# Kernel optimization log

Measured on AMD Instinct MI355X. Metric: run time of the kernel, lower is better.

The kernel has to match this reference:

```python
import jax, jax.numpy as jnp
import numpy as np

B, H, W, C_IN, C_HID = 32, 64, 64, 384, 128

def setup_inputs() -> dict:
    key = jax.random.key(0)
    k0, k1, k2 = jax.random.split(key, 3)
    dino_features = jax.random.normal(k0, (B, H, W, C_IN), dtype=jnp.float32)
    # Xavier-uniform(gain=0.5) bounds for conv weights, HWIO layout
    fan1 = C_IN * 9 + C_HID * 9
    lim1 = 0.5 * np.sqrt(6.0 / fan1)
    W1 = jax.random.uniform(k1, (3, 3, C_IN, C_HID), minval=-lim1, maxval=lim1, dtype=jnp.float32)
    b1 = jnp.zeros((C_HID,), dtype=jnp.float32)
    fan2 = C_HID + 1
    lim2 = 0.5 * np.sqrt(6.0 / fan2)
    W2 = jax.random.uniform(k2, (1, 1, C_HID, 1), minval=-lim2, maxval=lim2, dtype=jnp.float32)
    b2 = jnp.zeros((1,), dtype=jnp.float32)
    return {"dino_features": dino_features, "W1": W1, "b1": b1, "W2": W2, "b2": b2}

def _conv(x, w, pad):
    # x: NHWC, w: HWIO -> NHWC
    return jax.lax.conv_general_dilated(
        x, w, window_strides=(1, 1), padding=pad,
        dimension_numbers=("NHWC", "HWIO", "NHWC"))

def reference(dino_features, W1, b1, W2, b2):
    # conv3x3 (pad 1) -> ReLU -> conv1x1 -> sigmoid; output (B,H,W,1)
    h = jax.nn.relu(_conv(dino_features, W1, ((1, 1), (1, 1))) + b1)
    logits = _conv(h, W2, ((0, 0), (0, 0))) + b2
    return jax.nn.sigmoid(logits)
```

## Files before the change

kernel.cpp:

```cpp
#include <hip/hip_runtime.h>
#include <math.h>


typedef __attribute__((ext_vector_type(8))) unsigned short ushort8;
typedef __attribute__((ext_vector_type(8))) __bf16 bf16x8;
typedef __attribute__((ext_vector_type(4))) float floatx4;

static __device__ __forceinline__ unsigned short f2bf(float f) {
  union { float f; unsigned int u; } x; x.f = f;
  return (unsigned short)((x.u + 0x8000u) >> 16);
}
static __device__ __forceinline__ unsigned short f2bf_rne(float f) {
  union { float f; unsigned int u; } x; x.f = f;
  unsigned int u = x.u;
  return (unsigned short)((u + 0x7fffu + ((u >> 16) & 1u)) >> 16);
}

__global__ void prep_w1_kernel(const float* __restrict__ W1,
                               unsigned short* __restrict__ W1b) {
  __shared__ unsigned short tile[32 * 128];
  const int kk = blockIdx.x;
  const int o = kk / 12;
  const int chunk = kk - o * 12;
  const float* src = W1 + (o * 384 + chunk * 32) * 128;
  const int t = threadIdx.x;
#pragma unroll
  for (int i = 0; i < 16; ++i) {
    int idx = t + i * 256;
    int c = idx >> 7;
    int n = idx & 127;
    tile[n * 32 + c] = f2bf_rne(src[idx]);
  }
  __syncthreads();
  unsigned short* dst = W1b + kk * 4096;
#pragma unroll
  for (int i = 0; i < 16; ++i) {
    int idx = t + i * 256;
    dst[idx] = tile[idx];
  }
}

__global__ __launch_bounds__(256) void conv_fused_kernel(
    const float* __restrict__ x, const unsigned short* __restrict__ W1b,
    const float* __restrict__ b1, const float* __restrict__ W2,
    const float* __restrict__ b2, float* __restrict__ out) {
  __shared__ alignas(16) unsigned short Ah[100 * 40];
  __shared__ float hsum[64 * 4];

  const int t = threadIdx.x;
  const int w = t >> 6;
  const int lane = t & 63;
  const int g = lane >> 4;
  const int lr = lane & 15;

  const int img = blockIdx.x >> 6;
  const int tileId = blockIdx.x & 63;
  const int ty0 = (tileId >> 3) << 3;
  const int tx0 = (tileId & 7) << 3;

  const int px0 = t >> 2, sub0 = t & 3;
  const int hy0 = (px0 * 205) >> 11;
  const int hx0 = px0 - hy0 * 10;
  const int iy0 = ty0 + hy0 - 1, ix0 = tx0 + hx0 - 1;
  const bool v0 = ((unsigned)iy0 < 64u) && ((unsigned)ix0 < 64u);
  const float* ab0 =
      x + ((((img << 6) + iy0) << 6) + ix0) * 384 + sub0 * 8;

  const int i1 = t + 256;
  const bool act1 = i1 < 400;
  const int px1 = i1 >> 2, sub1 = i1 & 3;
  const int hy1 = (px1 * 205) >> 11;
  const int hx1 = px1 - hy1 * 10;
  const int iy1 = ty0 + hy1 - 1, ix1 = tx0 + hx1 - 1;
  const bool v1 = act1 && ((unsigned)iy1 < 64u) && ((unsigned)ix1 < 64u);
  const float* ab1 =
      x + ((((img << 6) + iy1) << 6) + ix1) * 384 + sub1 * 8;

  const int boff = ((w * 32 + lr) << 5) + (g << 3);
  const int aoffb = ((lr >> 3) * 10 + (lr & 7)) * 40 + (g << 3);

  floatx4 acc[4][2] = {};

  const float b1v0 = b1[w * 32 + lr];
  const float b1v1 = b1[w * 32 + 16 + lr];
  const float w2v0 = W2[w * 32 + lr];
  const float w2v1 = W2[w * 32 + 16 + lr];

  for (int chunk = 0; chunk < 12; ++chunk) {
    ushort8 a0 = (ushort8)0, a1 = (ushort8)0;
    if (v0) {
      const float* p = ab0 + (chunk << 5);
      float4 q0 = *(const float4*)p;
      float4 q1 = *(const float4*)(p + 4);
      a0[0] = f2bf(q0.x); a0[1] = f2bf(q0.y); a0[2] = f2bf(q0.z); a0[3] = f2bf(q0.w);
      a0[4] = f2bf(q1.x); a0[5] = f2bf(q1.y); a0[6] = f2bf(q1.z); a0[7] = f2bf(q1.w);
    }
    if (v1) {
      const float* p = ab1 + (chunk << 5);
      float4 q0 = *(const float4*)p;
      float4 q1 = *(const float4*)(p + 4);
      a1[0] = f2bf(q0.x); a1[1] = f2bf(q0.y); a1[2] = f2bf(q0.z); a1[3] = f2bf(q0.w);
      a1[4] = f2bf(q1.x); a1[5] = f2bf(q1.y); a1[6] = f2bf(q1.z); a1[7] = f2bf(q1.w);
    }

    __syncthreads();
    *(ushort8*)&Ah[px0 * 40 + sub0 * 8] = a0;
    if (act1) *(ushort8*)&Ah[px1 * 40 + sub1 * 8] = a1;
    __syncthreads();

#pragma unroll
    for (int o = 0; o < 9; ++o) {
      const int oy = o / 3, ox = o - oy * 3;
      const unsigned short* bp = W1b + ((o * 12 + chunk) << 12) + boff;
      bf16x8 bf0 = *(const bf16x8*)bp;
      bf16x8 bf1 = *(const bf16x8*)(bp + 512);
#pragma unroll
      for (int mi = 0; mi < 4; ++mi) {
        const bf16x8 af =
            *(const bf16x8*)&Ah[aoffb + (mi * 2 + oy) * 400 + ox * 40];
        acc[mi][0] = __builtin_amdgcn_mfma_f32_16x16x32_bf16(af, bf0, acc[mi][0], 0, 0, 0);
        acc[mi][1] = __builtin_amdgcn_mfma_f32_16x16x32_bf16(af, bf1, acc[mi][1], 0, 0, 0);
      }
    }
  }

#pragma unroll
  for (int mi = 0; mi < 4; ++mi) {
#pragma unroll
    for (int r = 0; r < 4; ++r) {
      float h0 = fmaxf(acc[mi][0][r] + b1v0, 0.0f);
      float h1 = fmaxf(acc[mi][1][r] + b1v1, 0.0f);
      float v = h0 * w2v0 + h1 * w2v1;
      v += __shfl_xor(v, 1);
      v += __shfl_xor(v, 2);
      v += __shfl_xor(v, 4);
      v += __shfl_xor(v, 8);
      if (lr == 0) {
        int m = mi * 16 + g * 4 + r;
        hsum[m * 4 + w] = v;
      }
    }
  }
  __syncthreads();
  if (t < 64) {
    float s = hsum[t * 4 + 0] + hsum[t * 4 + 1] + hsum[t * 4 + 2] +
              hsum[t * 4 + 3] + b2[0];
    float sig = 1.0f / (1.0f + expf(-s));
    int py = t >> 3, px = t & 7;
    out[((((img << 6) + ty0 + py) << 6) + tx0 + px)] = sig;
  }
}

extern "C" void kernel_launch(void* const* d_in, const int* in_sizes, int n_in,
                              void* d_out, int out_size, void* d_ws, size_t ws_size,
                              hipStream_t stream) {
  const float* x  = (const float*)d_in[0];
  const float* W1 = (const float*)d_in[1];
  const float* b1 = (const float*)d_in[2];
  const float* W2 = (const float*)d_in[3];
  const float* b2 = (const float*)d_in[4];
  float* out = (float*)d_out;
  unsigned short* W1b = (unsigned short*)d_ws;

  prep_w1_kernel<<<108, 256, 0, stream>>>(W1, W1b);
  conv_fused_kernel<<<2048, 256, 0, stream>>>(x, W1b, b1, W2, b2, out);
}
```

Measured before the change: 379.8 us.

## Enlarge conv tile to 8x16 with register-prefetched input and B-fragment reuse

Each block now computes an 8x16 output tile instead of 8x8, which cuts halo overhead (180 halo pixels for 128 outputs rather than 100 for 64) and halves the block count. The loop is reorganised so the three weight fragments for each kernel column are loaded once and reused across all tile rows, and each A fragment read from LDS feeds up to three MFMAs. Global loads for the next channel chunk are issued into registers before the current chunk's MFMAs, and conversion switches to the packed RNE bf16 intrinsic. In exchange, register use roughly doubles (16 accumulators plus 24 prefetch floats), which lowers occupancy, and there are fewer blocks to spread across the CUs.

```diff
diff --git a/kernel.cpp b/kernel.cpp
--- a/kernel.cpp
+++ b/kernel.cpp
@@ -1,4 +1,5 @@
 #include <hip/hip_runtime.h>
+#include <hip/hip_bf16.h>
 #include <math.h>
 
 
@@ -6,14 +7,23 @@
 typedef __attribute__((ext_vector_type(8))) __bf16 bf16x8;
 typedef __attribute__((ext_vector_type(4))) float floatx4;
 
-static __device__ __forceinline__ unsigned short f2bf(float f) {
-  union { float f; unsigned int u; } x; x.f = f;
-  return (unsigned short)((x.u + 0x8000u) >> 16);
-}
 static __device__ __forceinline__ unsigned short f2bf_rne(float f) {
   union { float f; unsigned int u; } x; x.f = f;
   unsigned int u = x.u;
   return (unsigned short)((u + 0x7fffu + ((u >> 16) & 1u)) >> 16);
+}
+
+static __device__ __forceinline__ ushort8 pack8(const float* v) {
+  ushort8 r;
+#pragma unroll
+  for (int i = 0; i < 4; ++i) {
+    __hip_bfloat162 p = __float22bfloat162_rn(make_float2(v[2 * i], v[2 * i + 1]));
+    union { __hip_bfloat162 b; unsigned int u; } c;
+    c.b = p;
+    r[2 * i] = (unsigned short)(c.u & 0xffffu);
+    r[2 * i + 1] = (unsigned short)(c.u >> 16);
+  }
+  return r;
 }
 
 __global__ void prep_w1_kernel(const float* __restrict__ W1,
@@ -44,8 +54,8 @@
     const float* __restrict__ x, const unsigned short* __restrict__ W1b,
     const float* __restrict__ b1, const float* __restrict__ W2,
     const float* __restrict__ b2, float* __restrict__ out) {
-  __shared__ alignas(16) unsigned short Ah[100 * 40];
-  __shared__ float hsum[64 * 4];
+  __shared__ alignas(16) unsigned short Ah[180 * 40];
+  __shared__ float hsum[128 * 4];
 
   const int t = threadIdx.x;
   const int w = t >> 6;
@@ -53,79 +63,100 @@
   const int g = lane >> 4;
   const int lr = lane & 15;
 
-  const int img = blockIdx.x >> 6;
-  const int tileId = blockIdx.x & 63;
-  const int ty0 = (tileId >> 3) << 3;
-  const int tx0 = (tileId & 7) << 3;
+  const int img = blockIdx.x >> 5;
+  const int tileId = blockIdx.x & 31;
+  const int ty0 = (tileId >> 2) << 3;
+  const int tx0 = (tileId & 3) << 4;
 
-  const int px0 = t >> 2, sub0 = t & 3;
-  const int hy0 = (px0 * 205) >> 11;
-  const int hx0 = px0 - hy0 * 10;
-  const int iy0 = ty0 + hy0 - 1, ix0 = tx0 + hx0 - 1;
-  const bool v0 = ((unsigned)iy0 < 64u) && ((unsigned)ix0 < 64u);
-  const float* ab0 =
-      x + ((((img << 6) + iy0) << 6) + ix0) * 384 + sub0 * 8;
-
-  const int i1 = t + 256;
-  const bool act1 = i1 < 400;
-  const int px1 = i1 >> 2, sub1 = i1 & 3;
-  const int hy1 = (px1 * 205) >> 11;
-  const int hx1 = px1 - hy1 * 10;
-  const int iy1 = ty0 + hy1 - 1, ix1 = tx0 + hx1 - 1;
-  const bool v1 = act1 && ((unsigned)iy1 < 64u) && ((unsigned)ix1 < 64u);
-  const float* ab1 =
-      x + ((((img << 6) + iy1) << 6) + ix1) * 384 + sub1 * 8;
+  int svalid[3];
+  const float* sptr[3];
+  int sloff[3];
+  const bool act2 = t < 208;
+#pragma unroll
+  for (int j = 0; j < 3; ++j) {
+    int i = t + j * 256;
+    int px = i >> 2, sub = i & 3;
+    int hy = (px * 57) >> 10;
+    int hx = px - hy * 18;
+    int iy = ty0 + hy - 1, ix = tx0 + hx - 1;
+    int v = ((unsigned)iy < 64u) && ((unsigned)ix < 64u);
+    if (j == 2 && !act2) v = 0;
+    svalid[j] = v;
+    int iyc = v ? iy : 0, ixc = v ? ix : 0;
+    sptr[j] = x + ((((img << 6) + iyc) << 6) + ixc) * 384 + sub * 8;
+    sloff[j] = px * 40 + sub * 8;
+  }
 
   const int boff = ((w * 32 + lr) << 5) + (g << 3);
-  const int aoffb = ((lr >> 3) * 10 + (lr & 7)) * 40 + (g << 3);
+  const int aoffl = lr * 40 + (g << 3);
 
-  floatx4 acc[4][2] = {};
+  floatx4 acc[8][2] = {};
 
   const float b1v0 = b1[w * 32 + lr];
   const float b1v1 = b1[w * 32 + 16 + lr];
   const float w2v0 = W2[w * 32 + lr];
   const float w2v1 = W2[w * 32 + 16 + lr];
 
+  float sreg[3][8];
+
+#pragma unroll
+  for (int j = 0; j < 3; ++j) {
+    if (svalid[j]) {
+      *(float4*)&sreg[j][0] = *(const float4*)sptr[j];
+      *(float4*)&sreg[j][4] = *(const float4*)(sptr[j] + 4);
+    } else {
+#pragma unroll
+      for (int e = 0; e < 8; ++e) sreg[j][e] = 0.0f;
+    }
+  }
+
   for (int chunk = 0; chunk < 12; ++chunk) {
-    ushort8 a0 = (ushort8)0, a1 = (ushort8)0;
-    if (v0) {
-      const float* p = ab0 + (chunk << 5);
-      float4 q0 = *(const float4*)p;
-      float4 q1 = *(const float4*)(p + 4);
-      a0[0] = f2bf(q0.x); a0[1] = f2bf(q0.y); a0[2] = f2bf(q0.z); a0[3] = f2bf(q0.w);
-      a0[4] = f2bf(q1.x); a0[5] = f2bf(q1.y); a0[6] = f2bf(q1.z); a0[7] = f2bf(q1.w);
-    }
-    if (v1) {
-      const float* p = ab1 + (chunk << 5);
-      float4 q0 = *(const float4*)p;
-      float4 q1 = *(const float4*)(p + 4);
-      a1[0] = f2bf(q0.x); a1[1] = f2bf(q0.y); a1[2] = f2bf(q0.z); a1[3] = f2bf(q0.w);
-      a1[4] = f2bf(q1.x); a1[5] = f2bf(q1.y); a1[6] = f2bf(q1.z); a1[7] = f2bf(q1.w);
+    __syncthreads();
+    *(ushort8*)&Ah[sloff[0]] = pack8(sreg[0]);
+    *(ushort8*)&Ah[sloff[1]] = pack8(sreg[1]);
+    if (act2) *(ushort8*)&Ah[sloff[2]] = pack8(sreg[2]);
+    __syncthreads();
+
+    if (chunk < 11) {
+      const int off = (chunk + 1) << 5;
+#pragma unroll
+      for (int j = 0; j < 3; ++j) {
+        if (svalid[j]) {
+          *(float4*)&sreg[j][0] = *(const float4*)(sptr[j] + off);
+          *(float4*)&sreg[j][4] = *(const float4*)(sptr[j] + off + 4);
+        }
+      }
     }
 
-    __syncthreads();
-    *(ushort8*)&Ah[px0 * 40 + sub0 * 8] = a0;
-    if (act1) *(ushort8*)&Ah[px1 * 40 + sub1 * 8] = a1;
-    __syncthreads();
-
 #pragma unroll
-    for (int o = 0; o < 9; ++o) {
-      const int oy = o / 3, ox = o - oy * 3;
-      const unsigned short* bp = W1b + ((o * 12 + chunk) << 12) + boff;
-      bf16x8 bf0 = *(const bf16x8*)bp;
-      bf16x8 bf1 = *(const bf16x8*)(bp + 512);
+    for (int ox = 0; ox < 3; ++ox) {
+      bf16x8 bf[3][2];
 #pragma unroll
-      for (int mi = 0; mi < 4; ++mi) {
-        const bf16x8 af =
-            *(const bf16x8*)&Ah[aoffb + (mi * 2 + oy) * 400 + ox * 40];
-        acc[mi][0] = __builtin_amdgcn_mfma_f32_16x16x32_bf16(af, bf0, acc[mi][0], 0, 0, 0);
-        acc[mi][1] = __builtin_amdgcn_mfma_f32_16x16x32_bf16(af, bf1, acc[mi][1], 0, 0, 0);
+      for (int oy = 0; oy < 3; ++oy) {
+        const unsigned short* bp =
+            W1b + ((((oy * 3 + ox) * 12 + chunk) << 12)) + boff;
+        bf[oy][0] = *(const bf16x8*)bp;
+        bf[oy][1] = *(const bf16x8*)(bp + 512);
+      }
+#pragma unroll
+      for (int h = 0; h < 10; ++h) {
+        const bf16x8 af = *(const bf16x8*)&Ah[h * 720 + ox * 40 + aoffl];
+#pragma unroll
+        for (int oy = 0; oy < 3; ++oy) {
+          const int mi = h - oy;
+          if (mi >= 0 && mi < 8) {
+            acc[mi][0] = __builtin_amdgcn_mfma_f32_16x16x32_bf16(
+                af, bf[oy][0], acc[mi][0], 0, 0, 0);
+            acc[mi][1] = __builtin_amdgcn_mfma_f32_16x16x32_bf16(
+                af, bf[oy][1], acc[mi][1], 0, 0, 0);
+          }
+        }
       }
     }
   }
 
 #pragma unroll
-  for (int mi = 0; mi < 4; ++mi) {
+  for (int mi = 0; mi < 8; ++mi) {
 #pragma unroll
     for (int r = 0; r < 4; ++r) {
       float h0 = fmaxf(acc[mi][0][r] + b1v0, 0.0f);
@@ -142,12 +173,12 @@
     }
   }
   __syncthreads();
-  if (t < 64) {
+  if (t < 128) {
     float s = hsum[t * 4 + 0] + hsum[t * 4 + 1] + hsum[t * 4 + 2] +
               hsum[t * 4 + 3] + b2[0];
     float sig = 1.0f / (1.0f + expf(-s));
-    int py = t >> 3, px = t & 7;
-    out[((((img << 6) + ty0 + py) << 6) + tx0 + px)] = sig;
+    int prow = t >> 4, pcol = t & 15;
+    out[((((img << 6) + ty0 + prow) << 6) + tx0 + pcol)] = sig;
   }
 }
 
@@ -163,5 +194,5 @@
   unsigned short* W1b = (unsigned short*)d_ws;
 
   prep_w1_kernel<<<108, 256, 0, stream>>>(W1, W1b);
-  conv_fused_kernel<<<2048, 256, 0, stream>>>(x, W1b, b1, W2, b2, out);
+  conv_fused_kernel<<<1024, 256, 0, stream>>>(x, W1b, b1, W2, b2, out);
 }
```

After: 346.6 us. 8.7% less time.
